# Optimization experiments

Hardware: AMD Instinct MI355X
Metric: run time of the kernel (lower is better)

Reference implementation:

```python
import jax, jax.numpy as jnp
import numpy as np

H = 16  # num_heads
B, N, M, D = 4, 512, 2048, 1024
FF = 4096  # mlp_ratio * D
LN_EPS = 1e-5


def _ln(x, g, b):
    m = x.mean(-1, keepdims=True)
    v = ((x - m) ** 2).mean(-1, keepdims=True)
    return (x - m) * jax.lax.rsqrt(v + LN_EPS) * g + b


def _attn(q_in, k_in, v_in, wq, bq, wk, bk, wv, bv, wp, bp):
    b, n, d = q_in.shape
    m = k_in.shape[1]
    hd = d // H
    scale = hd ** -0.5
    q = (q_in @ wq + bq).reshape(b, n, H, hd) * scale
    k = (k_in @ wk + bk).reshape(b, m, H, hd)
    v = (v_in @ wv + bv).reshape(b, m, H, hd)
    attn = jax.nn.softmax(jnp.einsum('bnhd,bmhd->bhnm', q, k), axis=-1)
    out = jnp.einsum('bhnm,bmhd->bnhd', attn, v).reshape(b, n, d)
    return out @ wp + bp


def setup_inputs() -> dict:
    key = jax.random.key(0)
    ks = iter(jax.random.split(key, 32))
    rnd = lambda shape: jax.random.normal(next(ks), shape, dtype=jnp.float32)
    w = lambda *shape: rnd(shape) * 0.02
    inp = {
        'state': rnd((B, N, D)),
        'patches': rnd((B, M, D)),
        'patches_pos_embed': rnd((B, M, D)),
        'state_query': rnd((B, N, D)),
    }
    for p in ('ca', 'sa'):
        inp[f'{p}_wq'] = w(D, D); inp[f'{p}_bq'] = jnp.zeros((D,), jnp.float32)
        inp[f'{p}_wk'] = w(D, D); inp[f'{p}_bk'] = jnp.zeros((D,), jnp.float32)
        inp[f'{p}_wv'] = w(D, D); inp[f'{p}_bv'] = jnp.zeros((D,), jnp.float32)
        inp[f'{p}_wp'] = w(D, D); inp[f'{p}_bp'] = jnp.zeros((D,), jnp.float32)
    inp['w1'] = w(D, FF); inp['b1'] = jnp.zeros((FF,), jnp.float32)
    inp['w2'] = w(FF, D); inp['b2'] = jnp.zeros((D,), jnp.float32)
    for i in (1, 2, 3):
        inp[f'n{i}_g'] = jnp.ones((D,), jnp.float32)
        inp[f'n{i}_b'] = jnp.zeros((D,), jnp.float32)
        inp[f'ls{i}'] = jnp.full((D,), 1e-5, jnp.float32)
    return inp


def reference(state, patches, patches_pos_embed, state_query,
              ca_wq, ca_bq, ca_wk, ca_bk, ca_wv, ca_bv, ca_wp, ca_bp,
              sa_wq, sa_bq, sa_wk, sa_bk, sa_wv, sa_bv, sa_wp, sa_bp,
              w1, b1, w2, b2,
              n1_g, n1_b, n2_g, n2_b, n3_g, n3_b,
              ls1, ls2, ls3):
    # pre-norm path of TransformerLayer.forward_pre (dropouts/drop_path = 0)
    state = state + state_query
    kv = patches + patches_pos_embed
    cross = _attn(_ln(state, n1_g, n1_b), kv, patches,
                  ca_wq, ca_bq, ca_wk, ca_bk, ca_wv, ca_bv, ca_wp, ca_bp)
    state = state + cross * ls1
    ns = _ln(state, n2_g, n2_b)
    selfa = _attn(ns, ns, ns,
                  sa_wq, sa_bq, sa_wk, sa_bk, sa_wv, sa_bv, sa_wp, sa_bp)
    state = state + selfa * ls2
    h = jax.nn.gelu(_ln(state, n3_g, n3_b) @ w1 + b1)
    return state + (h @ w2 + b2) * ls3
```

## Files before the change

### kernel.cpp

```cpp
#include <hip/hip_runtime.h>

#define DEV __device__ __forceinline__

typedef __bf16 bf16x8 __attribute__((ext_vector_type(8)));
typedef float f32x4 __attribute__((ext_vector_type(4)));

DEV unsigned short f2bf(float f) {
  __bf16 h = (__bf16)f;
  return __builtin_bit_cast(unsigned short, h);
}
DEV unsigned int cvtpk(float lo, float hi) {
  unsigned int r;
  asm("v_cvt_pk_bf16_f32 %0, %1, %2" : "=v"(r) : "v"(lo), "v"(hi));
  return r;
}

DEV void gload16(const void* g, void* l) {
  __builtin_amdgcn_global_load_lds(
      (const __attribute__((address_space(1))) unsigned int*)g,
      (__attribute__((address_space(3))) unsigned int*)l, 16, 0, 0);
}

DEV void tconv64_body(const float* __restrict__ W, unsigned short* __restrict__ Wt,
                      int K, int N, int bx, int by, float* tile ) {
  const int t = threadIdx.x;
  const int rr = t >> 4;
  const int cc = (t & 15) * 4;
#pragma unroll
  for (int it = 0; it < 4; it++) {
    float4 v = *reinterpret_cast<const float4*>(
        &W[(size_t)(by * 64 + it * 16 + rr) * N + bx * 64 + cc]);
    tile[(it * 16 + rr) * 65 + cc] = v.x;
    tile[(it * 16 + rr) * 65 + cc + 1] = v.y;
    tile[(it * 16 + rr) * 65 + cc + 2] = v.z;
    tile[(it * 16 + rr) * 65 + cc + 3] = v.w;
  }
  __syncthreads();
  const int nr = t >> 3;
  const int kc = (t & 7) * 8;
#pragma unroll
  for (int it = 0; it < 2; it++) {
    const int n = it * 32 + nr;
    uint4 o;
    o.x = cvtpk(tile[(kc + 0) * 65 + n], tile[(kc + 1) * 65 + n]);
    o.y = cvtpk(tile[(kc + 2) * 65 + n], tile[(kc + 3) * 65 + n]);
    o.z = cvtpk(tile[(kc + 4) * 65 + n], tile[(kc + 5) * 65 + n]);
    o.w = cvtpk(tile[(kc + 6) * 65 + n], tile[(kc + 7) * 65 + n]);
    *reinterpret_cast<uint4*>(&Wt[(size_t)(bx * 64 + n) * K + by * 64 + kc]) = o;
  }
}

DEV void add_ln_body(const float* __restrict__ a, const float* b, float* x0_out,
                     unsigned short* __restrict__ y, const float* __restrict__ gam,
                     const float* __restrict__ bet, int row) {
  const int t = threadIdx.x;
  const int c = t * 4;
  const size_t base = (size_t)row * 1024 + c;
  float4 v = *reinterpret_cast<const float4*>(a + base);
  if (b) {
    float4 v2 = *reinterpret_cast<const float4*>(b + base);
    v.x += v2.x; v.y += v2.y; v.z += v2.z; v.w += v2.w;
  }
  if (x0_out) *reinterpret_cast<float4*>(x0_out + base) = v;
  float s = v.x + v.y + v.z + v.w;
  float sq = v.x * v.x + v.y * v.y + v.z * v.z + v.w * v.w;
#pragma unroll
  for (int o = 32; o > 0; o >>= 1) {
    s += __shfl_xor(s, o);
    sq += __shfl_xor(sq, o);
  }
  __shared__ float ps[4], pq[4];
  const int w = t >> 6;
  if ((t & 63) == 0) { ps[w] = s; pq[w] = sq; }
  __syncthreads();
  s = ps[0] + ps[1] + ps[2] + ps[3];
  sq = pq[0] + pq[1] + pq[2] + pq[3];
  const float mean = s * (1.f / 1024.f);
  const float var = sq * (1.f / 1024.f) - mean * mean;
  const float rstd = rsqrtf(var + 1e-5f);
  float4 gv = *reinterpret_cast<const float4*>(gam + c);
  float4 bv = *reinterpret_cast<const float4*>(bet + c);
  uint2 o2;
  o2.x = cvtpk((v.x - mean) * rstd * gv.x + bv.x, (v.y - mean) * rstd * gv.y + bv.y);
  o2.y = cvtpk((v.z - mean) * rstd * gv.z + bv.z, (v.w - mean) * rstd * gv.w + bv.w);
  *reinterpret_cast<uint2*>(y + base) = o2;
}

DEV void kvcast_body4(const float* __restrict__ p, const float* __restrict__ pe,
                      unsigned short* __restrict__ kvo, unsigned short* __restrict__ po,
                      int bid) {
  float4 a[4], b[4];
  size_t idx[4];
#pragma unroll
  for (int it = 0; it < 4; it++) {
    idx[it] = ((size_t)bid * 256 + threadIdx.x + (size_t)it * 524288) * 4;
    a[it] = *reinterpret_cast<const float4*>(p + idx[it]);
    b[it] = *reinterpret_cast<const float4*>(pe + idx[it]);
  }
#pragma unroll
  for (int it = 0; it < 4; it++) {
    uint2 kv2, p2;
    kv2.x = cvtpk(a[it].x + b[it].x, a[it].y + b[it].y);
    kv2.y = cvtpk(a[it].z + b[it].z, a[it].w + b[it].w);
    p2.x = cvtpk(a[it].x, a[it].y);
    p2.y = cvtpk(a[it].z, a[it].w);
    *reinterpret_cast<uint2*>(kvo + idx[it]) = kv2;
    *reinterpret_cast<uint2*>(po + idx[it]) = p2;
  }
}

struct Pre {
  const float* caw[3]; unsigned short* cad[3];
  const float* state; const float* squery; float* stateF; unsigned short* lnB;
  const float* n1_g; const float* n1_b;
  const float* patches; const float* ppe; unsigned short* kvB; unsigned short* patB;
};
__global__ __launch_bounds__(256) void prelude_kernel(Pre p) {
  __shared__ __align__(16) float tile[64 * 65];
  const int bid = blockIdx.x;
  if (bid < 2048) {
    kvcast_body4(p.patches, p.ppe, p.kvB, p.patB, bid);
  } else if (bid < 2816) {
    const int i = bid - 2048;
    const int m = i >> 8, wi = i & 255;
    tconv64_body(p.caw[m], p.cad[m], 1024, 1024, wi & 15, wi >> 4, tile);
  } else {
    add_ln_body(p.state, p.squery, p.stateF, p.lnB, p.n1_g, p.n1_b, bid - 2816);
  }
}

__global__ __launch_bounds__(256) void add_ln_kernel(
    const float* __restrict__ a, const float* b, float* x0_out,
    unsigned short* __restrict__ y, const float* __restrict__ gam,
    const float* __restrict__ bet) {
  add_ln_body(a, b, x0_out, y, gam, bet, blockIdx.x);
}

DEV void xcd_swizzle(int gx, int gy, int& bx, int& by, int& bz) {
  const int gxy = gx * gy;
  const int nwg = gxy * gridDim.z;
  const int orig = (blockIdx.z * gy + blockIdx.y) * gx + blockIdx.x;
  const int q = nwg >> 3, r = nwg & 7;
  const int xcd = orig & 7;
  int wgid = (xcd < r ? xcd * (q + 1) : r * (q + 1) + (xcd - r) * q) + (orig >> 3);
  bz = wgid / gxy;
  wgid -= bz * gxy;
  if (gy >= gx) { by = wgid / gx; bx = wgid - by * gx; }
  else          { bx = wgid / gy; by = wgid - bx * gy; }
}

template <int BM, int BN>
DEV void gemm_core(const unsigned short* __restrict__ A,
                   const unsigned short* __restrict__ Bt,
                   unsigned short* As, unsigned short* Bs,
                   int brow, int bcol, int K, int lda, int koff,
                   f32x4 (&acc)[BM / 32][BN / 32]) {
  constexpr int WM = BM / 32, WN = BN / 32;
  const int t = threadIdx.x;
  const int lane = t & 63, w = t >> 6;
  const int wr = w >> 1, wc = w & 1;
  const int g = lane >> 4, lr = lane & 15;
  const int srow = lane >> 2, scol = (lane & 3) * 8;

  auto stage = [&](int buf, int k0) {
#pragma unroll
    for (int i = 0; i < BM / 64; i++) {
      const int r0 = (i * 4 + w) * 16;
      gload16(A + (size_t)(brow + r0 + srow) * lda + koff + k0 + scol,
              &As[buf * BM * 32 + r0 * 32]);
    }
#pragma unroll
    for (int i = 0; i < BN / 64; i++) {
      const int r0 = (i * 4 + w) * 16;
      gload16(Bt + (size_t)(bcol + r0 + srow) * lda + koff + k0 + scol,
              &Bs[buf * BN * 32 + r0 * 32]);
    }
  };

  stage(0, 0);
  const int nk = K / 32;
  int cur = 0;
  for (int kt = 0; kt < nk; kt++) {
    __syncthreads();
    if (kt + 1 < nk) stage(cur ^ 1, (kt + 1) * 32);
    bf16x8 af[WM], bfr[WN];
#pragma unroll
    for (int m = 0; m < WM; m++)
      af[m] = *reinterpret_cast<const bf16x8*>(
          &As[cur * BM * 32 + (wr * (BM / 2) + m * 16 + lr) * 32 + g * 8]);
#pragma unroll
    for (int n = 0; n < WN; n++)
      bfr[n] = *reinterpret_cast<const bf16x8*>(
          &Bs[cur * BN * 32 + (wc * (BN / 2) + n * 16 + lr) * 32 + g * 8]);
    __builtin_amdgcn_s_setprio(1);
#pragma unroll
    for (int m = 0; m < WM; m++)
#pragma unroll
      for (int n = 0; n < WN; n++)
        acc[m][n] = __builtin_amdgcn_mfma_f32_16x16x32_bf16(af[m], bfr[n], acc[m][n], 0, 0, 0);
    __builtin_amdgcn_s_setprio(0);
    cur ^= 1;
  }
}

template <int BM, int BN>
DEV void epilogue_vT(f32x4 (&acc)[BM / 32][BN / 32], unsigned short* smem,
                     unsigned short* __restrict__ vT, const float* __restrict__ bias,
                     int brow, int bcol, int vcol0, int vNk, int rpb) {
  constexpr int WM = BM / 32, WN = BN / 32;
  constexpr int LDT = 136;
  const int t = threadIdx.x, lane = t & 63, w = t >> 6;
  const int wr = w >> 1, wc = w & 1;
  const int g = lane >> 4, lr = lane & 15;
  __syncthreads();
#pragma unroll
  for (int m = 0; m < WM; m++) {
    const int row0 = wr * (BM / 2) + m * 16 + g * 4;
#pragma unroll
    for (int n = 0; n < WN; n++) {
      const int cc = wc * (BN / 2) + n * 16 + lr;
      const float bv = bias[bcol + cc];
      uint2 pk;
      pk.x = cvtpk(acc[m][n][0] + bv, acc[m][n][1] + bv);
      pk.y = cvtpk(acc[m][n][2] + bv, acc[m][n][3] + bv);
      *reinterpret_cast<uint2*>(&smem[cc * LDT + row0]) = pk;
    }
  }
  __syncthreads();
  const int b = brow / rpb;
  const int kvb = brow % rpb;
  constexpr int ITERS = BM * BN / (256 * 8);
#pragma unroll
  for (int it = 0; it < ITERS; it++) {
    const int idx = it * 256 + t;
    const int cc = idx / (BM / 8);
    const int ch = idx % (BM / 8);
    const int dg = bcol + cc - vcol0;
    const int h = dg >> 6, d = dg & 63;
    uint4 v = *reinterpret_cast<uint4*>(&smem[cc * LDT + ch * 8]);
    *reinterpret_cast<uint4*>(
        &vT[((size_t)(b * 16 + h) * 64 + d) * vNk + kvb + ch * 8]) = v;
  }
}

template <int EPI, int BM, int BN>
__global__ __launch_bounds__(256) void gemm_kernel(
    const unsigned short* __restrict__ A, const unsigned short* __restrict__ Bt,
    const float* __restrict__ bias, const float* resid,
    const float* __restrict__ ls, void* outp, int M, int N, int K, int lda,
    unsigned short* vT, int vcol0, int vNk, int rpb) {
  constexpr int WM = BM / 32;
  constexpr int WN = BN / 32;
  constexpr int STG = 2 * BM * 32 + 2 * BN * 32;
  constexpr int TRN = BN * 136;
  constexpr int SME = (EPI == 5 && TRN > STG) ? TRN : STG;
  __shared__ __align__(16) unsigned short smem[SME];
  unsigned short* As = smem;
  unsigned short* Bs = smem + 2 * BM * 32;
  const int t = threadIdx.x;
  const int lane = t & 63, w = t >> 6;
  const int wr = w >> 1, wc = w & 1;
  const int g = lane >> 4, lr = lane & 15;

  int bx, by, bz;
  xcd_swizzle(gridDim.x, gridDim.y, bx, by, bz);
  const int brow = by * BM, bcol = bx * BN;

  f32x4 acc[WM][WN] = {};
  gemm_core<BM, BN>(A, Bt, As, Bs, brow, bcol, K, lda, bz * K, acc);

  if (EPI == 5 && bcol >= vcol0) {
    epilogue_vT<BM, BN>(acc, smem, vT, bias, brow, bcol, vcol0, vNk, rpb);
    return;
  }

#pragma unroll
  for (int m = 0; m < WM; m++) {
    const int row0 = brow + wr * (BM / 2) + m * 16 + g * 4;
#pragma unroll
    for (int n = 0; n < WN; n++) {
      const int col = bcol + wc * (BN / 2) + n * 16 + lr;
      const float bv = (EPI == 4) ? 0.f : bias[col];
#pragma unroll
      for (int r = 0; r < 4; r++) {
        const float v = acc[m][n][r] + bv;
        const size_t idx = (size_t)(row0 + r) * N + col;
        if (EPI == 0 || EPI == 5) {
          ((unsigned short*)outp)[idx] = f2bf(v);
        } else if (EPI == 2) {
          ((float*)outp)[idx] = resid[idx] + v * ls[col];
        } else if (EPI == 3) {
          const float tth = tanhf(0.7978845608028654f * (v + 0.044715f * v * v * v));
          ((unsigned short*)outp)[idx] = f2bf(0.5f * v * (1.f + tth));
        } else {
          ((float*)outp)[(size_t)bz * M * N + idx] = v;
        }
      }
    }
  }
}

struct G3X {
  const unsigned short* A[3]; const unsigned short* Bt[3];
  const float* bias[3]; unsigned short* out[3]; int ecum[3];
  unsigned short* vT; int vNk; int rpb;
  const float* wp; unsigned short* wpt;
  const float* saw[4]; unsigned short* sad[4];
  const float* w1; unsigned short* w1t;
  const float* w2; unsigned short* w2t;
  const float* bq; const float* bk; const float* bv; float* bqkv;
};
__global__ __launch_bounds__(256) void gemm3_kernel(G3X p, int N, int K) {
  constexpr int BM = 128, BN = 128, WM = BM / 32, WN = BN / 32;
  constexpr int STG = 2 * BM * 32 + 2 * BN * 32;
  constexpr int TRN = BN * 136;
  constexpr int SME = (TRN > STG) ? TRN : STG;
  constexpr int NG = 1152;
  __shared__ __align__(16) unsigned short smem[SME];
  const int bid = blockIdx.x;
  const int t = threadIdx.x;

  if (bid >= NG) {
    float* tile = reinterpret_cast<float*>(smem);
    int i = bid - NG;
    if (i < 256) {
      tconv64_body(p.wp, p.wpt, 1024, 1024, i & 15, i >> 4, tile);
    } else if (i < 1280) {
      i -= 256;
      const int m = i >> 8, wi = i & 255;
      tconv64_body(p.saw[m], p.sad[m], 1024, 1024, wi & 15, wi >> 4, tile);
    } else if (i < 2304) {
      i -= 1280;
      tconv64_body(p.w1, p.w1t, 1024, 4096, i & 63, i >> 6, tile);
    } else if (i < 3328) {
      i -= 2304;
      tconv64_body(p.w2, p.w2t, 4096, 1024, i & 15, i >> 4, tile);
    } else {
      const int j = (i - 3328) * 256 + t;
      p.bqkv[j] = j < 1024 ? p.bq[j] : (j < 2048 ? p.bk[j - 1024] : p.bv[j - 2048]);
    }
    return;
  }

  unsigned short* As = smem;
  unsigned short* Bs = smem + 2 * BM * 32;
  const int lane = t & 63, w = t >> 6;
  const int wr = w >> 1, wc = w & 1;
  const int g = lane >> 4, lr = lane & 15;
  const int wgid = (bid & 7) * (NG >> 3) + (bid >> 3);
  const int by = wgid >> 3, bx = wgid & 7;
  const int s = (by >= p.ecum[0]) + (by >= p.ecum[1]);
  const int byloc = by - (s ? p.ecum[s - 1] : 0);
  const unsigned short* A = p.A[s];
  const unsigned short* Bt = p.Bt[s];
  const float* bias = p.bias[s];
  const int brow = byloc * BM, bcol = bx * BN;

  f32x4 acc[WM][WN] = {};
  gemm_core<BM, BN>(A, Bt, As, Bs, brow, bcol, K, K, 0, acc);

  if (s == 2) {
    epilogue_vT<BM, BN>(acc, smem, p.vT, bias, brow, bcol, 0, p.vNk, p.rpb);
    return;
  }
  unsigned short* outp = p.out[s];
#pragma unroll
  for (int m = 0; m < WM; m++) {
    const int row0 = brow + wr * (BM / 2) + m * 16 + g * 4;
#pragma unroll
    for (int n = 0; n < WN; n++) {
      const int col = bcol + wc * (BN / 2) + n * 16 + lr;
      const float bv = bias[col];
#pragma unroll
      for (int r = 0; r < 4; r++)
        outp[(size_t)(row0 + r) * N + col] = f2bf(acc[m][n][r] + bv);
    }
  }
}

__global__ __launch_bounds__(256) void splitk_red_kernel(
    const float* __restrict__ p, const float* __restrict__ bias,
    const float* __restrict__ resid, const float* __restrict__ ls,
    float* __restrict__ out) {
  const size_t i = ((size_t)blockIdx.x * 256 + threadIdx.x) * 4;
  const int c = (int)(i & 1023);
  float4 a = *reinterpret_cast<const float4*>(p + i);
  float4 b = *reinterpret_cast<const float4*>(p + 2048ull * 1024 + i);
  float4 rv = *reinterpret_cast<const float4*>(resid + i);
  float4 bb = *reinterpret_cast<const float4*>(bias + c);
  float4 lv = *reinterpret_cast<const float4*>(ls + c);
  float4 o;
  o.x = rv.x + (a.x + b.x + bb.x) * lv.x;
  o.y = rv.y + (a.y + b.y + bb.y) * lv.y;
  o.z = rv.z + (a.z + b.z + bb.z) * lv.z;
  o.w = rv.w + (a.w + b.w + bb.w) * lv.w;
  *reinterpret_cast<float4*>(out + i) = o;
}

__global__ __launch_bounds__(512) void attn_kernel(
    const unsigned short* __restrict__ Q, const unsigned short* __restrict__ Kp,
    const unsigned short* __restrict__ vT, unsigned short* __restrict__ O,
    int RSq, int RSk, int Nq, int Nk, float k2) {
  __shared__ __align__(16) unsigned short Ks[2][128 * 72];
  __shared__ __align__(16) unsigned short Vs[2][64 * 136];
  __shared__ __align__(16) unsigned short Ps[128 * 136];
  const int t = threadIdx.x, lane = t & 63, w = t >> 6;
  const int qt = blockIdx.y, h = blockIdx.x & 15, b = blockIdx.x >> 4;
  const int g = lane >> 4, lr = lane & 15;
  const int ksrow = t >> 2, kscol = (t & 3) * 16;
  const int vsrow = t >> 3, vscol = (t & 7) * 16;

  uint4 qr[2];
  {
    const unsigned short* qp = Q + (size_t)(b * Nq + qt * 128 + w * 16 + lr) * RSq + h * 64 + g * 8;
    qr[0] = *reinterpret_cast<const uint4*>(qp);
    qr[1] = *reinterpret_cast<const uint4*>(qp + 32);
  }
  float m_i = -1e30f, l_i = 0.f;
  f32x4 acc_o[4] = {};

  auto kaddr = [&](int kv0) {
    return reinterpret_cast<const uint4*>(
        Kp + (size_t)(b * Nk + kv0 + ksrow) * RSk + h * 64 + kscol);
  };
  auto vaddr = [&](int kv0) {
    return reinterpret_cast<const uint4*>(
        vT + ((size_t)(b * 16 + h) * 64 + vsrow) * Nk + kv0 + vscol);
  };

  uint4 kr0 = kaddr(0)[0], kr1 = kaddr(0)[1];
  uint4 vr0 = vaddr(0)[0], vr1 = vaddr(0)[1];

  int cur = 0;
  for (int kv0 = 0; kv0 < Nk; kv0 += 128) {
    *reinterpret_cast<uint4*>(&Ks[cur][ksrow * 72 + kscol]) = kr0;
    *reinterpret_cast<uint4*>(&Ks[cur][ksrow * 72 + kscol + 8]) = kr1;
    *reinterpret_cast<uint4*>(&Vs[cur][vsrow * 136 + vscol]) = vr0;
    *reinterpret_cast<uint4*>(&Vs[cur][vsrow * 136 + vscol + 8]) = vr1;
    __syncthreads();
    if (kv0 + 128 < Nk) {
      kr0 = kaddr(kv0 + 128)[0]; kr1 = kaddr(kv0 + 128)[1];
      vr0 = vaddr(kv0 + 128)[0]; vr1 = vaddr(kv0 + 128)[1];
    }

    f32x4 accs[8] = {};
    __builtin_amdgcn_s_setprio(1);
#pragma unroll
    for (int d0 = 0; d0 < 64; d0 += 32) {
      bf16x8 qf = __builtin_bit_cast(bf16x8, qr[d0 >> 5]);
#pragma unroll
      for (int m = 0; m < 8; m++) {
        bf16x8 kf = *reinterpret_cast<const bf16x8*>(&Ks[cur][(m * 16 + lr) * 72 + d0 + g * 8]);
        accs[m] = __builtin_amdgcn_mfma_f32_16x16x32_bf16(kf, qf, accs[m], 0, 0, 0);
      }
    }
    __builtin_amdgcn_s_setprio(0);
    float pmax = -1e30f;
#pragma unroll
    for (int m = 0; m < 8; m++)
#pragma unroll
      for (int r = 0; r < 4; r++) pmax = fmaxf(pmax, accs[m][r]);
    pmax = fmaxf(pmax, __shfl_xor(pmax, 16));
    pmax = fmaxf(pmax, __shfl_xor(pmax, 32));
    const float pm2 = pmax * k2;
    if (!__all(pm2 <= m_i + 8.f)) {
      const float m_new = fmaxf(m_i, pm2);
      const float corr = exp2f(m_i - m_new);
      m_i = m_new;
      l_i *= corr;
#pragma unroll
      for (int r = 0; r < 4; r++) {
        const float cf = __shfl(corr, g * 4 + r);
#pragma unroll
        for (int n = 0; n < 4; n++) acc_o[n][r] *= cf;
      }
    }
    float psum = 0.f;
#pragma unroll
    for (int m = 0; m < 8; m++) {
      float p0 = exp2f(fmaf(accs[m][0], k2, -m_i));
      float p1 = exp2f(fmaf(accs[m][1], k2, -m_i));
      float p2 = exp2f(fmaf(accs[m][2], k2, -m_i));
      float p3 = exp2f(fmaf(accs[m][3], k2, -m_i));
      psum += p0 + p1 + p2 + p3;
      uint2 pk;
      pk.x = cvtpk(p0, p1);
      pk.y = cvtpk(p2, p3);
      *reinterpret_cast<uint2*>(&Ps[(w * 16 + lr) * 136 + m * 16 + g * 4]) = pk;
    }
    psum += __shfl_xor(psum, 16);
    psum += __shfl_xor(psum, 32);
    l_i += psum;
    __builtin_amdgcn_s_setprio(1);
#pragma unroll
    for (int ks = 0; ks < 4; ks++) {
      bf16x8 pf = *reinterpret_cast<const bf16x8*>(&Ps[(w * 16 + lr) * 136 + ks * 32 + g * 8]);
#pragma unroll
      for (int n = 0; n < 4; n++) {
        bf16x8 vf = *reinterpret_cast<const bf16x8*>(&Vs[cur][(n * 16 + lr) * 136 + ks * 32 + g * 8]);
        acc_o[n] = __builtin_amdgcn_mfma_f32_16x16x32_bf16(pf, vf, acc_o[n], 0, 0, 0);
      }
    }
    __builtin_amdgcn_s_setprio(0);
    cur ^= 1;
  }
#pragma unroll
  for (int r = 0; r < 4; r++) {
    const float li = __shfl(l_i, g * 4 + r);
    const float inv = 1.f / li;
    const int qrow = qt * 128 + w * 16 + g * 4 + r;
#pragma unroll
    for (int n = 0; n < 4; n++)
      O[(size_t)(b * Nq + qrow) * 1024 + h * 64 + n * 16 + lr] = f2bf(acc_o[n][r] * inv);
  }
}

extern "C" void kernel_launch(void* const* d_in, const int* in_sizes, int n_in,
                              void* d_out, int out_size, void* d_ws, size_t ws_size,
                              hipStream_t stream) {
  const float* state = (const float*)d_in[0];
  const float* patches = (const float*)d_in[1];
  const float* ppe = (const float*)d_in[2];
  const float* squery = (const float*)d_in[3];
  const float* ca_wq = (const float*)d_in[4];
  const float* ca_bq = (const float*)d_in[5];
  const float* ca_wk = (const float*)d_in[6];
  const float* ca_bk = (const float*)d_in[7];
  const float* ca_wv = (const float*)d_in[8];
  const float* ca_bv = (const float*)d_in[9];
  const float* ca_wp = (const float*)d_in[10];
  const float* ca_bp = (const float*)d_in[11];
  const float* sa_wq = (const float*)d_in[12];
  const float* sa_bq = (const float*)d_in[13];
  const float* sa_wk = (const float*)d_in[14];
  const float* sa_bk = (const float*)d_in[15];
  const float* sa_wv = (const float*)d_in[16];
  const float* sa_bv = (const float*)d_in[17];
  const float* sa_wp = (const float*)d_in[18];
  const float* sa_bp = (const float*)d_in[19];
  const float* w1 = (const float*)d_in[20];
  const float* b1 = (const float*)d_in[21];
  const float* w2 = (const float*)d_in[22];
  const float* b2 = (const float*)d_in[23];
  const float* n1_g = (const float*)d_in[24];
  const float* n1_b = (const float*)d_in[25];
  const float* ls1 = (const float*)d_in[26];
  const float* n2_g = (const float*)d_in[27];
  const float* n2_b = (const float*)d_in[28];
  const float* ls2 = (const float*)d_in[29];
  const float* n3_g = (const float*)d_in[30];
  const float* n3_b = (const float*)d_in[31];
  const float* ls3 = (const float*)d_in[32];

  char* wsp = (char*)d_ws;
  auto alloc = [&](size_t bytes) {
    void* p = (void*)wsp;
    wsp += (bytes + 255) & ~(size_t)255;
    return p;
  };
  float* stateF = (float*)alloc(2048ull * 1024 * 4);
  unsigned short* lnB = (unsigned short*)alloc(2048ull * 1024 * 2);
  unsigned short* kvB = (unsigned short*)alloc(8192ull * 1024 * 2);
  unsigned short* patB = (unsigned short*)alloc(8192ull * 1024 * 2);
  unsigned short* qB = (unsigned short*)alloc(2048ull * 1024 * 2);
  unsigned short* kB = (unsigned short*)alloc(8192ull * 1024 * 2);
  unsigned short* vB = (unsigned short*)alloc(8192ull * 1024 * 2);
  unsigned short* oB = (unsigned short*)alloc(2048ull * 1024 * 2);
  unsigned short* hB = kvB;
  unsigned short* qkvB = kB;
  unsigned short* vTc = vB;
  unsigned short* vTs = qB;
  float* mlp2p = (float*)patB;
  unsigned short* ca_wqt = (unsigned short*)alloc(1024ull * 1024 * 2);
  unsigned short* ca_wkt = (unsigned short*)alloc(1024ull * 1024 * 2);
  unsigned short* ca_wvt = (unsigned short*)alloc(1024ull * 1024 * 2);
  unsigned short* ca_wpt = (unsigned short*)alloc(1024ull * 1024 * 2);
  unsigned short* sa_wqkvt = (unsigned short*)alloc(3072ull * 1024 * 2);
  unsigned short* sa_wpt = (unsigned short*)alloc(1024ull * 1024 * 2);
  unsigned short* w1t = (unsigned short*)alloc(4096ull * 1024 * 2);
  unsigned short* w2t = (unsigned short*)alloc(4096ull * 1024 * 2);
  float* sa_bqkv = (float*)alloc(3072 * 4);

  Pre pre;
  pre.caw[0] = ca_wq; pre.cad[0] = ca_wqt;
  pre.caw[1] = ca_wk; pre.cad[1] = ca_wkt;
  pre.caw[2] = ca_wv; pre.cad[2] = ca_wvt;
  pre.state = state; pre.squery = squery; pre.stateF = stateF; pre.lnB = lnB;
  pre.n1_g = n1_g; pre.n1_b = n1_b;
  pre.patches = patches; pre.ppe = ppe; pre.kvB = kvB; pre.patB = patB;
  prelude_kernel<<<4864, 256, 0, stream>>>(pre);

  const float k2 = 0.125f * 1.4426950408889634f;

  G3X g3;
  g3.A[0] = lnB;  g3.Bt[0] = ca_wqt; g3.bias[0] = ca_bq; g3.out[0] = qB;      g3.ecum[0] = 16;
  g3.A[1] = kvB;  g3.Bt[1] = ca_wkt; g3.bias[1] = ca_bk; g3.out[1] = kB;      g3.ecum[1] = 80;
  g3.A[2] = patB; g3.Bt[2] = ca_wvt; g3.bias[2] = ca_bv; g3.out[2] = nullptr; g3.ecum[2] = 144;
  g3.vT = vTc; g3.vNk = 2048; g3.rpb = 2048;
  g3.wp = ca_wp; g3.wpt = ca_wpt;
  g3.saw[0] = sa_wq; g3.sad[0] = sa_wqkvt;
  g3.saw[1] = sa_wk; g3.sad[1] = sa_wqkvt + 1024ull * 1024;
  g3.saw[2] = sa_wv; g3.sad[2] = sa_wqkvt + 2048ull * 1024;
  g3.saw[3] = sa_wp; g3.sad[3] = sa_wpt;
  g3.w1 = w1; g3.w1t = w1t; g3.w2 = w2; g3.w2t = w2t;
  g3.bq = sa_bq; g3.bk = sa_bk; g3.bv = sa_bv; g3.bqkv = sa_bqkv;
  gemm3_kernel<<<4492, 256, 0, stream>>>(g3, 1024, 1024);
  attn_kernel<<<dim3(64, 4), 512, 0, stream>>>(qB, kB, vTc, oB, 1024, 1024, 512, 2048, k2);
  gemm_kernel<2, 64, 64><<<dim3(16, 32), 256, 0, stream>>>(oB, ca_wpt, ca_bp, stateF, ls1, stateF, 2048, 1024, 1024, 1024, nullptr, 0, 0, 0);

  add_ln_kernel<<<2048, 256, 0, stream>>>(stateF, nullptr, nullptr, lnB, n2_g, n2_b);
  gemm_kernel<5, 128, 64><<<dim3(48, 16), 256, 0, stream>>>(lnB, sa_wqkvt, sa_bqkv, nullptr, nullptr, qkvB, 2048, 3072, 1024, 1024, vTs, 2048, 512, 512);
  attn_kernel<<<dim3(64, 4), 512, 0, stream>>>(qkvB, qkvB + 1024, vTs, oB, 3072, 3072, 512, 512, k2);
  gemm_kernel<2, 64, 64><<<dim3(16, 32), 256, 0, stream>>>(oB, sa_wpt, sa_bp, stateF, ls2, stateF, 2048, 1024, 1024, 1024, nullptr, 0, 0, 0);

  add_ln_kernel<<<2048, 256, 0, stream>>>(stateF, nullptr, nullptr, lnB, n3_g, n3_b);
  gemm_kernel<3, 128, 128><<<dim3(32, 16), 256, 0, stream>>>(lnB, w1t, b1, nullptr, nullptr, hB, 2048, 4096, 1024, 1024, nullptr, 0, 0, 0);
  gemm_kernel<4, 128, 64><<<dim3(16, 16, 2), 256, 0, stream>>>(hB, w2t, nullptr, nullptr, nullptr, mlp2p, 2048, 1024, 2048, 4096, nullptr, 0, 0, 0);
  splitk_red_kernel<<<2048, 256, 0, stream>>>(mlp2p, b2, stateF, ls3, (float*)d_out);
}
```

Before: 280.3 us.

## Interleave weight-transpose blocks with GEMM tiles and widen kv cast per thread

The kv/patch cast in the prelude now handles 8 contiguous floats per thread with 16-byte stores, using twice as many blocks instead of 4 strided float4s per thread. In the fused gemm3 kernel, weight-transpose and bias-copy blocks are interleaved with GEMM tiles (one GEMM tile in every four block IDs) instead of being appended after all GEMM tiles. The intent is to overlap memory-bound transpose work with compute-bound GEMM tiles across CUs and reduce tail imbalance. The grid grows slightly, adding a few idle blocks, and the XCD swizzle is recomputed from the compressed GEMM index.

Measured after the change: 393.0 us. 1.4x slower.

```diff
diff --git a/kernel.cpp b/kernel.cpp
--- a/kernel.cpp
+++ b/kernel.cpp
@@ -86,27 +86,25 @@
   *reinterpret_cast<uint2*>(y + base) = o2;
 }
 
-DEV void kvcast_body4(const float* __restrict__ p, const float* __restrict__ pe,
+DEV void kvcast_body8(const float* __restrict__ p, const float* __restrict__ pe,
                       unsigned short* __restrict__ kvo, unsigned short* __restrict__ po,
                       int bid) {
-  float4 a[4], b[4];
-  size_t idx[4];
-#pragma unroll
-  for (int it = 0; it < 4; it++) {
-    idx[it] = ((size_t)bid * 256 + threadIdx.x + (size_t)it * 524288) * 4;
-    a[it] = *reinterpret_cast<const float4*>(p + idx[it]);
-    b[it] = *reinterpret_cast<const float4*>(pe + idx[it]);
-  }
-#pragma unroll
-  for (int it = 0; it < 4; it++) {
-    uint2 kv2, p2;
-    kv2.x = cvtpk(a[it].x + b[it].x, a[it].y + b[it].y);
-    kv2.y = cvtpk(a[it].z + b[it].z, a[it].w + b[it].w);
-    p2.x = cvtpk(a[it].x, a[it].y);
-    p2.y = cvtpk(a[it].z, a[it].w);
-    *reinterpret_cast<uint2*>(kvo + idx[it]) = kv2;
-    *reinterpret_cast<uint2*>(po + idx[it]) = p2;
-  }
+  const size_t i = ((size_t)bid * 256 + threadIdx.x) * 8;
+  float4 a0 = *reinterpret_cast<const float4*>(p + i);
+  float4 a1 = *reinterpret_cast<const float4*>(p + i + 4);
+  float4 b0 = *reinterpret_cast<const float4*>(pe + i);
+  float4 b1 = *reinterpret_cast<const float4*>(pe + i + 4);
+  uint4 kv, pp;
+  kv.x = cvtpk(a0.x + b0.x, a0.y + b0.y);
+  kv.y = cvtpk(a0.z + b0.z, a0.w + b0.w);
+  kv.z = cvtpk(a1.x + b1.x, a1.y + b1.y);
+  kv.w = cvtpk(a1.z + b1.z, a1.w + b1.w);
+  pp.x = cvtpk(a0.x, a0.y);
+  pp.y = cvtpk(a0.z, a0.w);
+  pp.z = cvtpk(a1.x, a1.y);
+  pp.w = cvtpk(a1.z, a1.w);
+  *reinterpret_cast<uint4*>(kvo + i) = kv;
+  *reinterpret_cast<uint4*>(po + i) = pp;
 }
 
 struct Pre {
@@ -118,14 +116,14 @@
 __global__ __launch_bounds__(256) void prelude_kernel(Pre p) {
   __shared__ __align__(16) float tile[64 * 65];
   const int bid = blockIdx.x;
-  if (bid < 2048) {
-    kvcast_body4(p.patches, p.ppe, p.kvB, p.patB, bid);
-  } else if (bid < 2816) {
-    const int i = bid - 2048;
+  if (bid < 4096) {
+    kvcast_body8(p.patches, p.ppe, p.kvB, p.patB, bid);
+  } else if (bid < 4864) {
+    const int i = bid - 4096;
     const int m = i >> 8, wi = i & 255;
     tconv64_body(p.caw[m], p.cad[m], 1024, 1024, wi & 15, wi >> 4, tile);
   } else {
-    add_ln_body(p.state, p.squery, p.stateF, p.lnB, p.n1_g, p.n1_b, bid - 2816);
+    add_ln_body(p.state, p.squery, p.stateF, p.lnB, p.n1_g, p.n1_b, bid - 4864);
   }
 }
 
@@ -320,9 +318,9 @@
   const int bid = blockIdx.x;
   const int t = threadIdx.x;
 
-  if (bid >= NG) {
+  if (bid & 3) {
     float* tile = reinterpret_cast<float*>(smem);
-    int i = bid - NG;
+    int i = bid - (bid >> 2) - 1;
     if (i < 256) {
       tconv64_body(p.wp, p.wpt, 1024, 1024, i & 15, i >> 4, tile);
     } else if (i < 1280) {
@@ -335,7 +333,7 @@
     } else if (i < 3328) {
       i -= 2304;
       tconv64_body(p.w2, p.w2t, 4096, 1024, i & 15, i >> 4, tile);
-    } else {
+    } else if (i < 3340) {
       const int j = (i - 3328) * 256 + t;
       p.bqkv[j] = j < 1024 ? p.bq[j] : (j < 2048 ? p.bk[j - 1024] : p.bv[j - 2048]);
     }
@@ -347,7 +345,8 @@
   const int lane = t & 63, w = t >> 6;
   const int wr = w >> 1, wc = w & 1;
   const int g = lane >> 4, lr = lane & 15;
-  const int wgid = (bid & 7) * (NG >> 3) + (bid >> 3);
+  const int gid = bid >> 2;
+  const int wgid = (gid & 7) * (NG >> 3) + (gid >> 3);
   const int by = wgid >> 3, bx = wgid & 7;
   const int s = (by >= p.ecum[0]) + (by >= p.ecum[1]);
   const int byloc = by - (s ? p.ecum[s - 1] : 0);
@@ -588,7 +587,7 @@
   pre.state = state; pre.squery = squery; pre.stateF = stateF; pre.lnB = lnB;
   pre.n1_g = n1_g; pre.n1_b = n1_b;
   pre.patches = patches; pre.ppe = ppe; pre.kvB = kvB; pre.patB = patB;
-  prelude_kernel<<<4864, 256, 0, stream>>>(pre);
+  prelude_kernel<<<6912, 256, 0, stream>>>(pre);
 
   const float k2 = 0.125f * 1.4426950408889634f;
 
@@ -604,7 +603,7 @@
   g3.saw[3] = sa_wp; g3.sad[3] = sa_wpt;
   g3.w1 = w1; g3.w1t = w1t; g3.w2 = w2; g3.w2t = w2t;
   g3.bq = sa_bq; g3.bk = sa_bk; g3.bv = sa_bv; g3.bqkv = sa_bqkv;
-  gemm3_kernel<<<4492, 256, 0, stream>>>(g3, 1024, 1024);
+  gemm3_kernel<<<4608, 256, 0, stream>>>(g3, 1024, 1024);
   attn_kernel<<<dim3(64, 4), 512, 0, stream>>>(qB, kB, vTc, oB, 1024, 1024, 512, 2048, k2);
   gemm_kernel<2, 64, 64><<<dim3(16, 32), 256, 0, stream>>>(oB, ca_wpt, ca_bp, stateF, ls1, stateF, 2048, 1024, 1024, 1024, nullptr, 0, 0, 0);
 
```
